# Optimization experiments

Measured on AMD Instinct MI355X. Metric: run time of the kernel, lower is better.

## Reference

```python
import jax, jax.numpy as jnp
import numpy as np

K = 30          # hard-coded in Hypergraph.from_feature_kNN(ft, k=30)
BN_EPS = 1e-5   # BatchNorm1d eval mode, running_mean=0, running_var=1


def setup_inputs() -> dict:
    key = jax.random.key(0)
    ks = jax.random.split(key, 3)
    B, C, H, W = 8, 64, 56, 56
    hid = 32
    return {
        "x": jax.random.normal(ks[0], (B, C, H, W), jnp.float32),
        "w1": jax.random.normal(ks[1], (C, hid), jnp.float32) / np.sqrt(C).astype(np.float32),
        "b1": jnp.zeros((hid,), jnp.float32),
        "g1": jnp.ones((hid,), jnp.float32),
        "be1": jnp.zeros((hid,), jnp.float32),
        "w2": jax.random.normal(ks[2], (hid, C), jnp.float32) / np.sqrt(hid).astype(np.float32),
        "b2": jnp.zeros((C,), jnp.float32),
        "g2": jnp.ones((C,), jnp.float32),
        "be2": jnp.zeros((C,), jnp.float32),
    }


def _knn_idx(ft, k):
    # squared euclidean distances via gram trick; same ordering as torch.cdist
    sq = jnp.sum(ft * ft, axis=1)
    d2 = sq[:, None] + sq[None, :] - 2.0 * (ft @ ft.T)   # [L, L]
    _, idx = jax.lax.top_k(-d2, k)                        # k smallest distances (incl. self)
    return idx                                            # [L, k] -> hyperedge e = kNN of vertex e


def _v2v_mean(X, nbr):
    # hg.v2v(X, aggr="mean"): v2e mean then e2v mean over the kNN incidence structure
    L, k = nbr.shape
    F = X.shape[1]
    Y = jnp.mean(X[nbr], axis=1)                                        # v2e: [L_edges, F]
    seg = nbr.reshape(-1)                                               # vertex nbr[e,j] belongs to edge e
    vals = jnp.broadcast_to(Y[:, None, :], (L, k, F)).reshape(L * k, F)
    s = jax.ops.segment_sum(vals, seg, num_segments=L)                  # e2v sum
    dv = jax.ops.segment_sum(jnp.ones((L * k,), X.dtype), seg, num_segments=L)
    return s / jnp.maximum(dv, 1.0)[:, None]                            # e2v mean


def _bn_eval(x, g, b):
    # BatchNorm1d in eval: running_mean=0, running_var=1
    return x * (g * np.float32(1.0 / np.sqrt(1.0 + BN_EPS))) + b


def reference(x, w1, b1, g1, be1, w2, b2, g2, be2):
    B, C, H, W = x.shape
    L = H * W
    xf = x.reshape(B, L, C)  # faithful raw x.view(B, L, C) (no transpose in source)

    def per_sample(ft):
        nbr = _knn_idx(ft, K)
        # HGNNPConv 1: theta -> bn -> v2v(mean) -> relu (dropout off in eval)
        h = _bn_eval(ft @ w1 + b1, g1, be1)
        h = jax.nn.relu(_v2v_mean(h, nbr))
        # HGNNPConv 2 (is_last): theta -> bn -> v2v(mean), no act/drop
        h = _bn_eval(h @ w2 + b2, g2, be2)
        return _v2v_mean(h, nbr)  # [L, C]

    outs = jax.vmap(per_sample)(xf)      # [B, L, C]
    return outs.reshape(B, -1, H, W)     # faithful raw outs.view(B, -1, H, W)
```

## Files before the change

kernel.cpp:

```cpp
#include <hip/hip_runtime.h>
#include <math.h>


namespace {

constexpr int cB = 8;
constexpr int cL = 3136;
constexpr int cC = 64;
constexpr int cH = 32;
constexpr int cK = 30;
constexpr int NV = cB * cL;
constexpr int QD = 10;
constexpr float BN_SC = 0.99999500003749964f;

typedef __bf16 bf16x4 __attribute__((ext_vector_type(4)));
typedef __bf16 bf16x8 __attribute__((ext_vector_type(8)));
typedef float floatx4 __attribute__((ext_vector_type(4)));

__device__ inline unsigned umin2(unsigned a, unsigned b) { return a < b ? a : b; }
__device__ inline unsigned umax2(unsigned a, unsigned b) { return a > b ? a : b; }
__device__ inline unsigned umin3(unsigned a, unsigned b, unsigned c) {
  return umin2(umin2(a, b), c);
}
__device__ inline float bf16lo(unsigned u) { return __uint_as_float(u << 16); }
__device__ inline float bf16hi(unsigned u) {
  return __uint_as_float(u & 0xFFFF0000u);
}

__device__ inline unsigned bclean64(unsigned v, int ln) {
#pragma unroll
  for (int off = 32; off; off >>= 1) {
    unsigned p = (unsigned)__shfl_xor((int)v, off);
    v = (ln & off) ? umax2(v, p) : umin2(v, p);
  }
  return v;
}

__global__ void k_split(const float* __restrict__ x, ushort* __restrict__ xhi,
                        ushort* __restrict__ xlo, float* __restrict__ sqf,
                        int* __restrict__ cnt, int* __restrict__ cur) {
  int v = blockIdx.x * 256 + threadIdx.x;
  if (v >= NV) return;
  cnt[v] = 0;
  cur[v] = 0;
  const float4* p = reinterpret_cast<const float4*>(x) + (size_t)v * 16;
  double s = 0.0;
#pragma unroll
  for (int c = 0; c < 16; ++c) {
    float4 f = p[c];
    bf16x4 hh, ll;
#pragma unroll
    for (int e = 0; e < 4; ++e) {
      float a = (&f.x)[e];
      __bf16 h = (__bf16)a;
      ll[e] = (__bf16)(a - (float)h);
      hh[e] = h;
      s += (double)a * (double)a;
    }
    *reinterpret_cast<bf16x4*>(&xhi[(size_t)v * 64 + c * 4]) = hh;
    *reinterpret_cast<bf16x4*>(&xlo[(size_t)v * 64 + c * 4]) = ll;
  }
  sqf[v] = (float)(s * 1024.0 + 262144.0);
}

__global__ __launch_bounds__(128, 4) void k_sweep(
    const ushort* __restrict__ xhi, const ushort* __restrict__ xlo,
    const float* __restrict__ sqf, unsigned* __restrict__ candq) {
  const int ib = blockIdx.x, qt = blockIdx.y, b = blockIdx.z;
  const int r0 = ib * 32;
  const int jb0 = qt * 1568;
  const int ntile = 49;
  const size_t bbase = (size_t)b * cL;

  __shared__ ushort aHi[32 * 72], aLo[32 * 72];
  __shared__ ushort bHi[32 * 72], bLo[32 * 72];
  __shared__ float sqJs[32];

  const int t  = threadIdx.x;
  const int ln = t & 63;
  const int w  = t >> 6;
  const int tx = ln & 15;
  const int qd = ln >> 4;

#pragma unroll
  for (int it = 0; it < 2; ++it) {
    int idx = t + 128 * it;
    int r = idx >> 3, blk = idx & 7;
    *reinterpret_cast<uint4*>(&aHi[r * 72 + blk * 8]) =
        *reinterpret_cast<const uint4*>(&xhi[(bbase + r0 + r) * 64 + blk * 8]);
    *reinterpret_cast<uint4*>(&aLo[r * 72 + blk * 8]) =
        *reinterpret_cast<const uint4*>(&xlo[(bbase + r0 + r) * 64 + blk * 8]);
  }
  __syncthreads();

  bf16x8 aH[2], aL[2];
#pragma unroll
  for (int kk = 0; kk < 2; ++kk) {
    aH[kk] = *reinterpret_cast<const bf16x8*>(
        &aHi[(w * 16 + tx) * 72 + kk * 32 + qd * 8]);
    aL[kk] = *reinterpret_cast<const bf16x8*>(
        &aLo[(w * 16 + tx) * 72 + kk * 32 + qd * 8]);
  }

  unsigned q[4][QD];
#pragma unroll
  for (int e = 0; e < 4; ++e)
#pragma unroll
    for (int k = 0; k < QD; ++k) q[e][k] = 0xFFFFFFFFu;

  const int pr  = (t + 0)   >> 3, pblk  = (t + 0)   & 7;
  const int pr1 = (t + 128) >> 3, pblk1 = (t + 128) & 7;
  uint4 pH0, pH1, pL0, pL1;
  float pS = 0.f;
  {
    const int jb = jb0;
    pH0 = *reinterpret_cast<const uint4*>(&xhi[(bbase + jb + pr) * 64 + pblk * 8]);
    pL0 = *reinterpret_cast<const uint4*>(&xlo[(bbase + jb + pr) * 64 + pblk * 8]);
    pH1 = *reinterpret_cast<const uint4*>(&xhi[(bbase + jb + pr1) * 64 + pblk1 * 8]);
    pL1 = *reinterpret_cast<const uint4*>(&xlo[(bbase + jb + pr1) * 64 + pblk1 * 8]);
    if (t < 32) pS = sqf[bbase + jb + t];
  }

  for (int st = 0; st < ntile; ++st) {
    __syncthreads();
    *reinterpret_cast<uint4*>(&bHi[pr * 72 + pblk * 8])   = pH0;
    *reinterpret_cast<uint4*>(&bLo[pr * 72 + pblk * 8])   = pL0;
    *reinterpret_cast<uint4*>(&bHi[pr1 * 72 + pblk1 * 8]) = pH1;
    *reinterpret_cast<uint4*>(&bLo[pr1 * 72 + pblk1 * 8]) = pL1;
    if (t < 32) sqJs[t] = pS;
    __syncthreads();

    if (st + 1 < ntile) {
      const int jb = jb0 + (st + 1) * 32;
      pH0 = *reinterpret_cast<const uint4*>(&xhi[(bbase + jb + pr) * 64 + pblk * 8]);
      pL0 = *reinterpret_cast<const uint4*>(&xlo[(bbase + jb + pr) * 64 + pblk * 8]);
      pH1 = *reinterpret_cast<const uint4*>(&xhi[(bbase + jb + pr1) * 64 + pblk1 * 8]);
      pL1 = *reinterpret_cast<const uint4*>(&xlo[(bbase + jb + pr1) * 64 + pblk1 * 8]);
      if (t < 32) pS = sqf[bbase + jb + t];
    }
    __builtin_amdgcn_sched_barrier(0);

    unsigned pk[2][4];
#pragma unroll
    for (int f = 0; f < 2; ++f) {
      const int bro = (f * 16 + tx) * 72 + qd * 8;
      bf16x8 bh0 = *reinterpret_cast<const bf16x8*>(&bHi[bro]);
      bf16x8 bh1 = *reinterpret_cast<const bf16x8*>(&bHi[bro + 32]);
      bf16x8 bl0 = *reinterpret_cast<const bf16x8*>(&bLo[bro]);
      bf16x8 bl1 = *reinterpret_cast<const bf16x8*>(&bLo[bro + 32]);
      floatx4 acc = {0.f, 0.f, 0.f, 0.f};
      acc = __builtin_amdgcn_mfma_f32_16x16x32_bf16(aH[0], bh0, acc, 0, 0, 0);
      acc = __builtin_amdgcn_mfma_f32_16x16x32_bf16(aH[1], bh1, acc, 0, 0, 0);
      acc = __builtin_amdgcn_mfma_f32_16x16x32_bf16(aH[0], bl0, acc, 0, 0, 0);
      acc = __builtin_amdgcn_mfma_f32_16x16x32_bf16(aH[1], bl1, acc, 0, 0, 0);
      acc = __builtin_amdgcn_mfma_f32_16x16x32_bf16(aL[0], bh0, acc, 0, 0, 0);
      acc = __builtin_amdgcn_mfma_f32_16x16x32_bf16(aL[1], bh1, acc, 0, 0, 0);
      const float sjs = sqJs[f * 16 + tx];
      const unsigned col = (unsigned)(jb0 + st * 32 + f * 16 + tx);
#pragma unroll
      for (int e = 0; e < 4; ++e) {
        float qf = fmaf(acc[e], -2048.f, sjs);
        qf = fminf(fmaxf(qf, 0.f), 1048575.f);
        pk[f][e] = ((unsigned)qf << 12) | col;
      }
    }

#pragma unroll
    for (int e = 0; e < 4; ++e) {
      unsigned a0 = umin2(pk[0][e], pk[1][e]);
      unsigned a1 = umax2(pk[0][e], pk[1][e]);
      if (__any(a0 < q[e][QD - 1])) {
#pragma unroll
        for (int i = QD - 1; i >= 2; --i)
          q[e][i] = umin3(q[e][i], umax2(q[e][i - 1], a0),
                          umax2(q[e][i - 2], a1));
        q[e][1] = umin3(q[e][1], umax2(q[e][0], a0), a1);
        q[e][0] = umin3(q[e][0], a0, a1);
      }
    }
  }

  unsigned* cr[4];
#pragma unroll
  for (int e = 0; e < 4; ++e)
    cr[e] = candq + (bbase + r0 + w * 16 + qd * 4 + e) * 80 + qt * 40;
  for (int it = 0; it < 40; ++it) {
    unsigned h0 = q[0][0], h1 = q[1][0], h2 = q[2][0], h3 = q[3][0];
    unsigned m0 = h0, m1 = h1, m2 = h2, m3 = h3;
#pragma unroll
    for (int off = 1; off < 16; off <<= 1) {
      m0 = umin2(m0, (unsigned)__shfl_xor((int)m0, off));
      m1 = umin2(m1, (unsigned)__shfl_xor((int)m1, off));
      m2 = umin2(m2, (unsigned)__shfl_xor((int)m2, off));
      m3 = umin2(m3, (unsigned)__shfl_xor((int)m3, off));
    }
    if (tx == 0) {
      cr[0][it] = m0;
      cr[1][it] = m1;
      cr[2][it] = m2;
      cr[3][it] = m3;
    }
    if (h0 == m0) {
#pragma unroll
      for (int k = 0; k < QD - 1; ++k) q[0][k] = q[0][k + 1];
      q[0][QD - 1] = 0xFFFFFFFFu;
    }
    if (h1 == m1) {
#pragma unroll
      for (int k = 0; k < QD - 1; ++k) q[1][k] = q[1][k + 1];
      q[1][QD - 1] = 0xFFFFFFFFu;
    }
    if (h2 == m2) {
#pragma unroll
      for (int k = 0; k < QD - 1; ++k) q[2][k] = q[2][k + 1];
      q[2][QD - 1] = 0xFFFFFFFFu;
    }
    if (h3 == m3) {
#pragma unroll
      for (int k = 0; k < QD - 1; ++k) q[3][k] = q[3][k + 1];
      q[3][QD - 1] = 0xFFFFFFFFu;
    }
  }
}

__global__ __launch_bounds__(256) void k_rescore(const float* __restrict__ x,
                                                 const unsigned* __restrict__ candq,
                                                 int* __restrict__ nbr,
                                                 int* __restrict__ cnt) {
  const int w  = threadIdx.x >> 6;
  const int ln = threadIdx.x & 63;
  const size_t row = (size_t)blockIdx.x * 4 + w;
  const size_t bvert = row - (row % cL);

  const unsigned* cq = candq + row * 80;
  unsigned A = (ln < 40) ? cq[ln]      : 0xFFFFFFFFu;
  unsigned B = (ln < 40) ? cq[40 + ln] : 0xFFFFFFFFu;

  unsigned g = umin2(A, (unsigned)__shfl((int)B, 63 - ln));
  g = bclean64(g, ln);

  const unsigned qv = g >> 12;
  const int col = min((int)(g & 0xFFFu), cL - 1);

  unsigned q29 = (unsigned)__shfl((int)qv, 29);
  unsigned q30 = (unsigned)__shfl((int)qv, 30);
  if (q30 > q29 + 6) {
    if (ln < cK) {
      nbr[row * cK + ln] = col;
      atomicAdd(&cnt[bvert + col], 1);
    }
    return;
  }

  float4 xi[16];
  const float4* xi4 = reinterpret_cast<const float4*>(x + row * 64);
#pragma unroll
  for (int c = 0; c < 16; ++c) xi[c] = xi4[c];

  double dv = 1e300;
  if (ln < 40) {
    const float4* xj4 = reinterpret_cast<const float4*>(x + (bvert + col) * 64);
    double ax = 0.0, ay = 0.0, az = 0.0, aw = 0.0;
#pragma unroll
    for (int c = 0; c < 16; ++c) {
      float4 xj = xj4[c];
      double d0 = (double)xi[c].x - (double)xj.x; ax = fma(d0, d0, ax);
      double d1 = (double)xi[c].y - (double)xj.y; ay = fma(d1, d1, ay);
      double d2 = (double)xi[c].z - (double)xj.z; az = fma(d2, d2, az);
      double d3 = (double)xi[c].w - (double)xj.w; aw = fma(d3, d3, aw);
    }
    dv = (ax + ay) + (az + aw);
  }
  int r2 = 0;
  for (int j = 0; j < 40; ++j) {
    double od = __shfl(dv, j);
    r2 += (od < dv || (od == dv && j < ln)) ? 1 : 0;
  }
  if (ln < 40 && r2 < cK) {
    nbr[row * cK + r2] = col;
    atomicAdd(&cnt[bvert + col], 1);
  }
}

__global__ __launch_bounds__(1024) void k_scan(const int* __restrict__ cnt,
                                               int* __restrict__ rp) {
  const int b = blockIdx.x;
  const int* c = cnt + b * cL;
  int* r = rp + b * (cL + 1);
  const int t = threadIdx.x;
  const int ln = t & 63, w = t >> 6;

  int v[4];
  int s = 0;
#pragma unroll
  for (int i = 0; i < 4; ++i) {
    int idx = 4 * t + i;
    v[i] = (idx < cL) ? c[idx] : 0;
    s += v[i];
  }
  int inc = s;
#pragma unroll
  for (int off = 1; off < 64; off <<= 1) {
    int u = __shfl_up(inc, off);
    if (ln >= off) inc += u;
  }
  __shared__ int wsum[16];
  if (ln == 63) wsum[w] = inc;
  __syncthreads();
  int carry = 0;
#pragma unroll
  for (int i = 0; i < 16; ++i) carry += (i < w) ? wsum[i] : 0;

  int excl = carry + inc - s;
#pragma unroll
  for (int i = 0; i < 4; ++i) {
    int idx = 4 * t + i;
    if (idx < cL) r[idx] = excl;
    excl += v[i];
  }
  if (t == 1023) r[cL] = excl;
}

__global__ void k_fill(const int* __restrict__ nbr, const int* __restrict__ rp,
                       int* __restrict__ cur, int* __restrict__ el) {
  int g = blockIdx.x * 256 + threadIdx.x;
  if (g >= NV * cK) return;
  int b = g / (cL * cK);
  int e = (g / cK) % cL;
  int v = nbr[g];
  v = min(max(v, 0), cL - 1);
  int p = rp[b * (cL + 1) + v] + atomicAdd(&cur[b * cL + v], 1);
  p = min(max(p, 0), cL * cK - 1);
  el[(size_t)b * cL * cK + p] = e;
}

__global__ __launch_bounds__(256) void k_theta1(const float* __restrict__ x,
                                                const float* __restrict__ w1,
                                                const float* __restrict__ b1,
                                                const float* __restrict__ g1,
                                                const float* __restrict__ be1,
                                                __bf16* __restrict__ h1) {
  __shared__ float w[cC * cH];
  int t = threadIdx.x;
  for (int n = t; n < cC * cH; n += 256) w[n] = w1[n];
  __syncthreads();
  int g = blockIdx.x * 256 + t;
  int row = g >> 5;
  int f = g & 31;
  const float4* xr = reinterpret_cast<const float4*>(x) + (size_t)row * 16;
  float s = 0.f;
#pragma unroll
  for (int kc = 0; kc < 16; ++kc) {
    float4 xv = xr[kc];
    s += xv.x * w[(4 * kc + 0) * cH + f];
    s += xv.y * w[(4 * kc + 1) * cH + f];
    s += xv.z * w[(4 * kc + 2) * cH + f];
    s += xv.w * w[(4 * kc + 3) * cH + f];
  }
  h1[g] = (__bf16)((s + b1[f]) * (g1[f] * BN_SC) + be1[f]);
}

__global__ __launch_bounds__(256) void k_v2e32(const __bf16* __restrict__ X,
                                               const int* __restrict__ nbr,
                                               __bf16* __restrict__ Y) {
  const int w  = threadIdx.x >> 6;
  const int ln = threadIdx.x & 63;
  const size_t er = (size_t)blockIdx.x * 4 + w;
  const size_t b  = er / cL;
  const unsigned* Xb = reinterpret_cast<const unsigned*>(X + b * cL * cH);
  const int nb_l = nbr[er * cK + (ln < cK ? ln : cK - 1)];
  const int qg = ln >> 4, f2 = ln & 15;
  unsigned u[8];
#pragma unroll
  for (int m = 0; m < 8; ++m) {
    int j = m * 4 + qg;
    int idx = __shfl(nb_l, j < cK ? j : 0);
    u[m] = Xb[(size_t)idx * 16 + f2];
  }
  float s0 = 0.f, s1 = 0.f;
#pragma unroll
  for (int m = 0; m < 8; ++m) {
    bool ok = (m * 4 + qg) < cK;
    s0 += ok ? bf16lo(u[m]) : 0.f;
    s1 += ok ? bf16hi(u[m]) : 0.f;
  }
  s0 += __shfl_xor(s0, 16);
  s1 += __shfl_xor(s1, 16);
  s0 += __shfl_xor(s0, 32);
  s1 += __shfl_xor(s1, 32);
  if (ln < 16) {
    union {
      __bf16 h[2];
      unsigned u;
    } cv;
    cv.h[0] = (__bf16)(s0 * (1.f / 30.f));
    cv.h[1] = (__bf16)(s1 * (1.f / 30.f));
    reinterpret_cast<unsigned*>(Y)[er * 16 + f2] = cv.u;
  }
}

__global__ __launch_bounds__(256) void k_e2v_t2(const __bf16* __restrict__ Y,
                                                const int* __restrict__ rp,
                                                const int* __restrict__ el,
                                                const float* __restrict__ w2,
                                                const float* __restrict__ b2,
                                                const float* __restrict__ g2,
                                                const float* __restrict__ be2,
                                                __bf16* __restrict__ h2) {
  __shared__ float w2s[cH * cC];
  {
    int t = threadIdx.x;
    for (int n = t; n < cH * cC; n += 256) w2s[n] = w2[n];
  }
  const int w  = threadIdx.x >> 6;
  const int ln = threadIdx.x & 63;
  const size_t vr = (size_t)blockIdx.x * 4 + w;
  const size_t b  = vr / cL;
  const int v = (int)(vr % cL);
  const int* rpb = rp + b * (cL + 1);
  const int s0 = rpb[v];
  const int deg = rpb[v + 1] - s0;
  const int* elb = el + b * (size_t)cL * cK + s0;
  const __bf16* Yb = Y + b * cL * cH;
  const int hi = ln >> 5, f = ln & 31;
  float s = 0.f;

  for (int base = 0; base < deg; base += 64) {
    const int take = min(64, deg - base);
    const int eidx = elb[base + (ln < take ? ln : 0)];
    for (int j0 = 0; j0 < take; j0 += 16) {
      float acc = 0.f;
#pragma unroll
      for (int k2 = 0; k2 < 8; ++k2) {
        int j = j0 + 2 * k2 + hi;
        int e0 = __shfl(eidx, j < take ? j : 0);
        float y = (float)Yb[(size_t)e0 * cH + f];
        acc += (j < take) ? y : 0.f;
      }
      s += acc;
    }
  }
  __syncthreads();

  s += __shfl_xor(s, 32);
  float r = fmaxf(s / (float)deg, 0.f);

  float s2 = 0.f;
#pragma unroll 8
  for (int k = 0; k < cH; ++k) {
    float rk = __shfl(r, k);
    s2 = fmaf(rk, w2s[k * cC + ln], s2);
  }
  h2[vr * cC + ln] = (__bf16)((s2 + b2[ln]) * (g2[ln] * BN_SC) + be2[ln]);
}

__global__ __launch_bounds__(256) void k_v2e64(const __bf16* __restrict__ X,
                                               const int* __restrict__ nbr,
                                               __bf16* __restrict__ Y) {
  const int w  = threadIdx.x >> 6;
  const int ln = threadIdx.x & 63;
  const size_t er = (size_t)blockIdx.x * 4 + w;
  const size_t b  = er / cL;
  const unsigned* Xb = reinterpret_cast<const unsigned*>(X + b * cL * cC);
  const int nb_l = nbr[er * cK + (ln < cK ? ln : cK - 1)];
  const int half = ln >> 5, f2 = ln & 31;
  int idx[15];
#pragma unroll
  for (int m = 0; m < 15; ++m) idx[m] = __shfl(nb_l, 2 * m + half);
  unsigned v[15];
#pragma unroll
  for (int m = 0; m < 15; ++m) v[m] = Xb[(size_t)idx[m] * 32 + f2];
  float s0 = 0.f, s1 = 0.f;
#pragma unroll
  for (int m = 0; m < 15; ++m) {
    s0 += bf16lo(v[m]);
    s1 += bf16hi(v[m]);
  }
  s0 += __shfl_xor(s0, 32);
  s1 += __shfl_xor(s1, 32);
  if (half == 0) {
    union {
      __bf16 h[2];
      unsigned u;
    } cv;
    cv.h[0] = (__bf16)(s0 * (1.f / 30.f));
    cv.h[1] = (__bf16)(s1 * (1.f / 30.f));
    reinterpret_cast<unsigned*>(Y)[er * 32 + f2] = cv.u;
  }
}

__global__ __launch_bounds__(256) void k_e2v64(const __bf16* __restrict__ Y,
                                               const int* __restrict__ rp,
                                               const int* __restrict__ el,
                                               float* __restrict__ out) {
  const int w  = threadIdx.x >> 6;
  const int ln = threadIdx.x & 63;
  const size_t vr = (size_t)blockIdx.x * 4 + w;
  const size_t b  = vr / cL;
  const int v = (int)(vr % cL);
  const int* rpb = rp + b * (cL + 1);
  const int s0r = rpb[v];
  const int deg = rpb[v + 1] - s0r;
  const int* elb = el + b * (size_t)cL * cK + s0r;
  const unsigned* Yb = reinterpret_cast<const unsigned*>(Y + b * cL * cC);
  const int half = ln >> 5, f2 = ln & 31;
  float s0 = 0.f, s1 = 0.f;

  for (int base = 0; base < deg; base += 64) {
    const int take = min(64, deg - base);
    const int eidx = elb[base + (ln < take ? ln : 0)];
    for (int j0 = 0; j0 < take; j0 += 16) {
      float a0 = 0.f, a1 = 0.f;
#pragma unroll
      for (int k2 = 0; k2 < 8; ++k2) {
        int j = j0 + 2 * k2 + half;
        int e0 = __shfl(eidx, j < take ? j : 0);
        unsigned u = Yb[(size_t)e0 * 32 + f2];
        bool ok = j < take;
        a0 += ok ? bf16lo(u) : 0.f;
        a1 += ok ? bf16hi(u) : 0.f;
      }
      s0 += a0;
      s1 += a1;
    }
  }
  s0 += __shfl_xor(s0, 32);
  s1 += __shfl_xor(s1, 32);
  float v0 = __shfl(s0, ln >> 1);
  float v1 = __shfl(s1, ln >> 1);
  out[vr * cC + ln] = ((ln & 1) ? v1 : v0) / (float)deg;
}

}

extern "C" void kernel_launch(void* const* d_in, const int* in_sizes, int n_in,
                              void* d_out, int out_size, void* d_ws,
                              size_t ws_size, hipStream_t stream) {
  (void)in_sizes; (void)n_in; (void)out_size; (void)ws_size;
  const float* x   = (const float*)d_in[0];
  const float* w1  = (const float*)d_in[1];
  const float* b1  = (const float*)d_in[2];
  const float* g1  = (const float*)d_in[3];
  const float* be1 = (const float*)d_in[4];
  const float* w2  = (const float*)d_in[5];
  const float* b2  = (const float*)d_in[6];
  const float* g2  = (const float*)d_in[7];
  const float* be2 = (const float*)d_in[8];
  float* out = (float*)d_out;

  char* base = (char*)d_ws;
  size_t off = 0;
  auto carve = [&](size_t bytes) {
    char* p = base + off;
    off += (bytes + 255) & ~(size_t)255;
    return p;
  };
  float* sqf = (float*)carve((size_t)NV * 4);
  int*   nbr = (int*)carve((size_t)NV * cK * 4);
  int*   rp  = (int*)carve((size_t)cB * (cL + 1) * 4);
  int*   cnt = (int*)carve((size_t)NV * 4);
  int*   cur = (int*)carve((size_t)NV * 4);
  char* RA = carve((size_t)NV * 64 * 2 * 2);
  ushort* xhi = (ushort*)RA;
  ushort* xlo = (ushort*)(RA + 3211264);
  int* el = (int*)RA;
  char* RC = carve((size_t)NV * 160 * 4);
  unsigned* candq = (unsigned*)RC;
  __bf16* h1 = (__bf16*)RC;
  __bf16* Y1 = (__bf16*)(RC + 1605632);
  __bf16* h2 = (__bf16*)(RC + 3211264);
  __bf16* Y2 = (__bf16*)(RC + 6422528);

  k_split<<<(NV + 255) / 256, 256, 0, stream>>>(x, xhi, xlo, sqf, cnt, cur);
  k_sweep<<<dim3(98, 2, cB), 128, 0, stream>>>(xhi, xlo, sqf, candq);
  k_rescore<<<NV / 4, 256, 0, stream>>>(x, candq, nbr, cnt);

  k_scan<<<cB, 1024, 0, stream>>>(cnt, rp);
  k_fill<<<(NV * cK) / 256, 256, 0, stream>>>(nbr, rp, cur, el);

  k_theta1<<<NV * cH / 256, 256, 0, stream>>>(x, w1, b1, g1, be1, h1);
  k_v2e32<<<NV / 4, 256, 0, stream>>>(h1, nbr, Y1);
  k_e2v_t2<<<NV / 4, 256, 0, stream>>>(Y1, rp, el, w2, b2, g2, be2, h2);
  k_v2e64<<<NV / 4, 256, 0, stream>>>(h2, nbr, Y2);
  k_e2v64<<<NV / 4, 256, 0, stream>>>(Y2, rp, el, out);
}
```

Before: 389.7 us.

## Fuse split with theta1, fold v2e32 into rescore, drop LDS staging in kNN sweep

```diff
diff --git a/kernel.cpp b/kernel.cpp
--- a/kernel.cpp
+++ b/kernel.cpp
@@ -13,9 +13,13 @@
 constexpr int QD = 10;
 constexpr float BN_SC = 0.99999500003749964f;
 
-typedef __bf16 bf16x4 __attribute__((ext_vector_type(4)));
 typedef __bf16 bf16x8 __attribute__((ext_vector_type(8)));
 typedef float floatx4 __attribute__((ext_vector_type(4)));
+
+union BU {
+  __bf16 b[2];
+  unsigned u;
+};
 
 __device__ inline unsigned umin2(unsigned a, unsigned b) { return a < b ? a : b; }
 __device__ inline unsigned umax2(unsigned a, unsigned b) { return a > b ? a : b; }
@@ -36,71 +40,62 @@
   return v;
 }
 
-__global__ void k_split(const float* __restrict__ x, ushort* __restrict__ xhi,
-                        ushort* __restrict__ xlo, float* __restrict__ sqf,
-                        int* __restrict__ cnt, int* __restrict__ cur) {
-  int v = blockIdx.x * 256 + threadIdx.x;
-  if (v >= NV) return;
-  cnt[v] = 0;
-  cur[v] = 0;
-  const float4* p = reinterpret_cast<const float4*>(x) + (size_t)v * 16;
-  double s = 0.0;
-#pragma unroll
-  for (int c = 0; c < 16; ++c) {
-    float4 f = p[c];
-    bf16x4 hh, ll;
-#pragma unroll
-    for (int e = 0; e < 4; ++e) {
-      float a = (&f.x)[e];
-      __bf16 h = (__bf16)a;
-      ll[e] = (__bf16)(a - (float)h);
-      hh[e] = h;
-      s += (double)a * (double)a;
-    }
-    *reinterpret_cast<bf16x4*>(&xhi[(size_t)v * 64 + c * 4]) = hh;
-    *reinterpret_cast<bf16x4*>(&xlo[(size_t)v * 64 + c * 4]) = ll;
-  }
-  sqf[v] = (float)(s * 1024.0 + 262144.0);
-}
-
-__global__ __launch_bounds__(128, 4) void k_sweep(
+__global__ __launch_bounds__(256) void k_splitth(
+    const float* __restrict__ x, const float* __restrict__ w1,
+    const float* __restrict__ b1, const float* __restrict__ g1,
+    const float* __restrict__ be1, ushort* __restrict__ xhi,
+    ushort* __restrict__ xlo, float* __restrict__ sqf,
+    int* __restrict__ cnt, int* __restrict__ cur, __bf16* __restrict__ h1) {
+  __shared__ float w1s[cC * cH];
+  __shared__ float xs[8 * 64];
+  const int t = threadIdx.x;
+  const int v0 = blockIdx.x * 8;
+  for (int n = t; n < cC * cH; n += 256) w1s[n] = w1[n];
+  {
+    float2 xv = reinterpret_cast<const float2*>(x + (size_t)v0 * 64)[t];
+    xs[2 * t] = xv.x;
+    xs[2 * t + 1] = xv.y;
+    BU hh, ll;
+    hh.b[0] = (__bf16)xv.x;
+    hh.b[1] = (__bf16)xv.y;
+    ll.b[0] = (__bf16)(xv.x - (float)hh.b[0]);
+    ll.b[1] = (__bf16)(xv.y - (float)hh.b[1]);
+    reinterpret_cast<unsigned*>(xhi)[(size_t)v0 * 32 + t] = hh.u;
+    reinterpret_cast<unsigned*>(xlo)[(size_t)v0 * 32 + t] = ll.u;
+    float ss = xv.x * xv.x + xv.y * xv.y;
+#pragma unroll
+    for (int off = 1; off < 32; off <<= 1) ss += __shfl_xor(ss, off);
+    if ((t & 31) == 0) sqf[v0 + (t >> 5)] = ss * 1024.f + 262144.f;
+  }
+  if (t < 8) {
+    cnt[v0 + t] = 0;
+    cur[v0 + t] = 0;
+  }
+  __syncthreads();
+  const int r = t >> 5, f = t & 31;
+  float s = 0.f;
+#pragma unroll
+  for (int k = 0; k < cC; ++k) s = fmaf(xs[r * 64 + k], w1s[k * cH + f], s);
+  h1[(size_t)(v0 + r) * cH + f] =
+      (__bf16)((s + b1[f]) * (g1[f] * BN_SC) + be1[f]);
+}
+
+__global__ __launch_bounds__(64, 4) void k_sweep(
     const ushort* __restrict__ xhi, const ushort* __restrict__ xlo,
     const float* __restrict__ sqf, unsigned* __restrict__ candq) {
   const int ib = blockIdx.x, qt = blockIdx.y, b = blockIdx.z;
-  const int r0 = ib * 32;
+  const int r0 = ib * 16;
   const int jb0 = qt * 1568;
-  const int ntile = 49;
   const size_t bbase = (size_t)b * cL;
-
-  __shared__ ushort aHi[32 * 72], aLo[32 * 72];
-  __shared__ ushort bHi[32 * 72], bLo[32 * 72];
-  __shared__ float sqJs[32];
-
-  const int t  = threadIdx.x;
-  const int ln = t & 63;
-  const int w  = t >> 6;
+  const int ln = threadIdx.x;
   const int tx = ln & 15;
   const int qd = ln >> 4;
 
-#pragma unroll
-  for (int it = 0; it < 2; ++it) {
-    int idx = t + 128 * it;
-    int r = idx >> 3, blk = idx & 7;
-    *reinterpret_cast<uint4*>(&aHi[r * 72 + blk * 8]) =
-        *reinterpret_cast<const uint4*>(&xhi[(bbase + r0 + r) * 64 + blk * 8]);
-    *reinterpret_cast<uint4*>(&aLo[r * 72 + blk * 8]) =
-        *reinterpret_cast<const uint4*>(&xlo[(bbase + r0 + r) * 64 + blk * 8]);
-  }
-  __syncthreads();
-
-  bf16x8 aH[2], aL[2];
-#pragma unroll
-  for (int kk = 0; kk < 2; ++kk) {
-    aH[kk] = *reinterpret_cast<const bf16x8*>(
-        &aHi[(w * 16 + tx) * 72 + kk * 32 + qd * 8]);
-    aL[kk] = *reinterpret_cast<const bf16x8*>(
-        &aLo[(w * 16 + tx) * 72 + kk * 32 + qd * 8]);
-  }
+  const size_t aoff = (bbase + r0 + tx) * 64 + qd * 8;
+  const bf16x8 aH0 = *reinterpret_cast<const bf16x8*>(&xhi[aoff]);
+  const bf16x8 aH1 = *reinterpret_cast<const bf16x8*>(&xhi[aoff + 32]);
+  const bf16x8 aL0 = *reinterpret_cast<const bf16x8*>(&xlo[aoff]);
+  const bf16x8 aL1 = *reinterpret_cast<const bf16x8*>(&xlo[aoff + 32]);
 
   unsigned q[4][QD];
 #pragma unroll
@@ -108,82 +103,70 @@
 #pragma unroll
     for (int k = 0; k < QD; ++k) q[e][k] = 0xFFFFFFFFu;
 
-  const int pr  = (t + 0)   >> 3, pblk  = (t + 0)   & 7;
-  const int pr1 = (t + 128) >> 3, pblk1 = (t + 128) & 7;
-  uint4 pH0, pH1, pL0, pL1;
-  float pS = 0.f;
-  {
-    const int jb = jb0;
-    pH0 = *reinterpret_cast<const uint4*>(&xhi[(bbase + jb + pr) * 64 + pblk * 8]);
-    pL0 = *reinterpret_cast<const uint4*>(&xlo[(bbase + jb + pr) * 64 + pblk * 8]);
-    pH1 = *reinterpret_cast<const uint4*>(&xhi[(bbase + jb + pr1) * 64 + pblk1 * 8]);
-    pL1 = *reinterpret_cast<const uint4*>(&xlo[(bbase + jb + pr1) * 64 + pblk1 * 8]);
-    if (t < 32) pS = sqf[bbase + jb + t];
-  }
-
-  for (int st = 0; st < ntile; ++st) {
-    __syncthreads();
-    *reinterpret_cast<uint4*>(&bHi[pr * 72 + pblk * 8])   = pH0;
-    *reinterpret_cast<uint4*>(&bLo[pr * 72 + pblk * 8])   = pL0;
-    *reinterpret_cast<uint4*>(&bHi[pr1 * 72 + pblk1 * 8]) = pH1;
-    *reinterpret_cast<uint4*>(&bLo[pr1 * 72 + pblk1 * 8]) = pL1;
-    if (t < 32) sqJs[t] = pS;
-    __syncthreads();
-
-    if (st + 1 < ntile) {
-      const int jb = jb0 + (st + 1) * 32;
-      pH0 = *reinterpret_cast<const uint4*>(&xhi[(bbase + jb + pr) * 64 + pblk * 8]);
-      pL0 = *reinterpret_cast<const uint4*>(&xlo[(bbase + jb + pr) * 64 + pblk * 8]);
-      pH1 = *reinterpret_cast<const uint4*>(&xhi[(bbase + jb + pr1) * 64 + pblk1 * 8]);
-      pL1 = *reinterpret_cast<const uint4*>(&xlo[(bbase + jb + pr1) * 64 + pblk1 * 8]);
-      if (t < 32) pS = sqf[bbase + jb + t];
-    }
-    __builtin_amdgcn_sched_barrier(0);
-
-    unsigned pk[2][4];
-#pragma unroll
-    for (int f = 0; f < 2; ++f) {
-      const int bro = (f * 16 + tx) * 72 + qd * 8;
-      bf16x8 bh0 = *reinterpret_cast<const bf16x8*>(&bHi[bro]);
-      bf16x8 bh1 = *reinterpret_cast<const bf16x8*>(&bHi[bro + 32]);
-      bf16x8 bl0 = *reinterpret_cast<const bf16x8*>(&bLo[bro]);
-      bf16x8 bl1 = *reinterpret_cast<const bf16x8*>(&bLo[bro + 32]);
-      floatx4 acc = {0.f, 0.f, 0.f, 0.f};
-      acc = __builtin_amdgcn_mfma_f32_16x16x32_bf16(aH[0], bh0, acc, 0, 0, 0);
-      acc = __builtin_amdgcn_mfma_f32_16x16x32_bf16(aH[1], bh1, acc, 0, 0, 0);
-      acc = __builtin_amdgcn_mfma_f32_16x16x32_bf16(aH[0], bl0, acc, 0, 0, 0);
-      acc = __builtin_amdgcn_mfma_f32_16x16x32_bf16(aH[1], bl1, acc, 0, 0, 0);
-      acc = __builtin_amdgcn_mfma_f32_16x16x32_bf16(aL[0], bh0, acc, 0, 0, 0);
-      acc = __builtin_amdgcn_mfma_f32_16x16x32_bf16(aL[1], bh1, acc, 0, 0, 0);
-      const float sjs = sqJs[f * 16 + tx];
-      const unsigned col = (unsigned)(jb0 + st * 32 + f * 16 + tx);
-#pragma unroll
-      for (int e = 0; e < 4; ++e) {
-        float qf = fmaf(acc[e], -2048.f, sjs);
-        qf = fminf(fmaxf(qf, 0.f), 1048575.f);
-        pk[f][e] = ((unsigned)qf << 12) | col;
-      }
-    }
-
+  const ushort* ph0 = xhi + (bbase + jb0 + tx) * 64 + qd * 8;
+  const ushort* ph1 = ph0 + 16 * 64;
+  const ushort* pl0 = xlo + (bbase + jb0 + tx) * 64 + qd * 8;
+  const ushort* pl1 = pl0 + 16 * 64;
+  const float* ps = sqf + bbase + jb0 + tx;
+
+  for (int st = 0; st < 49; ++st) {
+    bf16x8 b0h0 = *reinterpret_cast<const bf16x8*>(ph0);
+    bf16x8 b0h1 = *reinterpret_cast<const bf16x8*>(ph0 + 32);
+    bf16x8 b0l0 = *reinterpret_cast<const bf16x8*>(pl0);
+    bf16x8 b0l1 = *reinterpret_cast<const bf16x8*>(pl0 + 32);
+    bf16x8 b1h0 = *reinterpret_cast<const bf16x8*>(ph1);
+    bf16x8 b1h1 = *reinterpret_cast<const bf16x8*>(ph1 + 32);
+    bf16x8 b1l0 = *reinterpret_cast<const bf16x8*>(pl1);
+    bf16x8 b1l1 = *reinterpret_cast<const bf16x8*>(pl1 + 32);
+    const float sj0 = ps[0];
+    const float sj1 = ps[16];
+
+    floatx4 acc0 = {0.f, 0.f, 0.f, 0.f};
+    acc0 = __builtin_amdgcn_mfma_f32_16x16x32_bf16(aH0, b0h0, acc0, 0, 0, 0);
+    acc0 = __builtin_amdgcn_mfma_f32_16x16x32_bf16(aH1, b0h1, acc0, 0, 0, 0);
+    acc0 = __builtin_amdgcn_mfma_f32_16x16x32_bf16(aH0, b0l0, acc0, 0, 0, 0);
+    acc0 = __builtin_amdgcn_mfma_f32_16x16x32_bf16(aH1, b0l1, acc0, 0, 0, 0);
+    acc0 = __builtin_amdgcn_mfma_f32_16x16x32_bf16(aL0, b0h0, acc0, 0, 0, 0);
+    acc0 = __builtin_amdgcn_mfma_f32_16x16x32_bf16(aL1, b0h1, acc0, 0, 0, 0);
+    floatx4 acc1 = {0.f, 0.f, 0.f, 0.f};
+    acc1 = __builtin_amdgcn_mfma_f32_16x16x32_bf16(aH0, b1h0, acc1, 0, 0, 0);
+    acc1 = __builtin_amdgcn_mfma_f32_16x16x32_bf16(aH1, b1h1, acc1, 0, 0, 0);
+    acc1 = __builtin_amdgcn_mfma_f32_16x16x32_bf16(aH0, b1l0, acc1, 0, 0, 0);
+    acc1 = __builtin_amdgcn_mfma_f32_16x16x32_bf16(aH1, b1l1, acc1, 0, 0, 0);
+    acc1 = __builtin_amdgcn_mfma_f32_16x16x32_bf16(aL0, b1h0, acc1, 0, 0, 0);
+    acc1 = __builtin_amdgcn_mfma_f32_16x16x32_bf16(aL1, b1h1, acc1, 0, 0, 0);
+
+    const unsigned col0 = (unsigned)(jb0 + st * 32 + tx);
+    unsigned pk0[4], pk1[4];
 #pragma unroll
     for (int e = 0; e < 4; ++e) {
-      unsigned a0 = umin2(pk[0][e], pk[1][e]);
-      unsigned a1 = umax2(pk[0][e], pk[1][e]);
-      if (__any(a0 < q[e][QD - 1])) {
-#pragma unroll
-        for (int i = QD - 1; i >= 2; --i)
-          q[e][i] = umin3(q[e][i], umax2(q[e][i - 1], a0),
-                          umax2(q[e][i - 2], a1));
-        q[e][1] = umin3(q[e][1], umax2(q[e][0], a0), a1);
-        q[e][0] = umin3(q[e][0], a0, a1);
-      }
-    }
+      float q0 = fmaf(acc0[e], -2048.f, sj0);
+      q0 = fminf(fmaxf(q0, 0.f), 1048575.f);
+      pk0[e] = ((unsigned)q0 << 12) | col0;
+      float q1 = fmaf(acc1[e], -2048.f, sj1);
+      q1 = fminf(fmaxf(q1, 0.f), 1048575.f);
+      pk1[e] = ((unsigned)q1 << 12) | (col0 + 16);
+    }
+
+#pragma unroll
+    for (int e = 0; e < 4; ++e) {
+      unsigned a0 = umin2(pk0[e], pk1[e]);
+      unsigned a1 = umax2(pk0[e], pk1[e]);
+#pragma unroll
+      for (int i = QD - 1; i >= 2; --i)
+        q[e][i] = umin3(q[e][i], umax2(q[e][i - 1], a0),
+                        umax2(q[e][i - 2], a1));
+      q[e][1] = umin3(q[e][1], umax2(q[e][0], a0), a1);
+      q[e][0] = umin3(q[e][0], a0, a1);
+    }
+
+    ph0 += 2048; ph1 += 2048; pl0 += 2048; pl1 += 2048; ps += 32;
   }
 
   unsigned* cr[4];
 #pragma unroll
   for (int e = 0; e < 4; ++e)
-    cr[e] = candq + (bbase + r0 + w * 16 + qd * 4 + e) * 80 + qt * 40;
+    cr[e] = candq + (bbase + r0 + qd * 4 + e) * 80 + qt * 40;
   for (int it = 0; it < 40; ++it) {
     unsigned h0 = q[0][0], h1 = q[1][0], h2 = q[2][0], h3 = q[3][0];
     unsigned m0 = h0, m1 = h1, m2 = h2, m3 = h3;
@@ -223,10 +206,10 @@
   }
 }
 
-__global__ __launch_bounds__(256) void k_rescore(const float* __restrict__ x,
-                                                 const unsigned* __restrict__ candq,
-                                                 int* __restrict__ nbr,
-                                                 int* __restrict__ cnt) {
+__global__ __launch_bounds__(256) void k_rescore(
+    const float* __restrict__ x, const unsigned* __restrict__ candq,
+    const __bf16* __restrict__ h1, int* __restrict__ nbr,
+    int* __restrict__ cnt, __bf16* __restrict__ Y1) {
   const int w  = threadIdx.x >> 6;
   const int ln = threadIdx.x & 63;
   const size_t row = (size_t)blockIdx.x * 4 + w;
@@ -244,41 +227,60 @@
 
   unsigned q29 = (unsigned)__shfl((int)qv, 29);
   unsigned q30 = (unsigned)__shfl((int)qv, 30);
-  if (q30 > q29 + 6) {
-    if (ln < cK) {
-      nbr[row * cK + ln] = col;
-      atomicAdd(&cnt[bvert + col], 1);
-    }
-    return;
-  }
-
-  float4 xi[16];
-  const float4* xi4 = reinterpret_cast<const float4*>(x + row * 64);
-#pragma unroll
-  for (int c = 0; c < 16; ++c) xi[c] = xi4[c];
-
-  double dv = 1e300;
-  if (ln < 40) {
-    const float4* xj4 = reinterpret_cast<const float4*>(x + (bvert + col) * 64);
-    double ax = 0.0, ay = 0.0, az = 0.0, aw = 0.0;
-#pragma unroll
-    for (int c = 0; c < 16; ++c) {
-      float4 xj = xj4[c];
-      double d0 = (double)xi[c].x - (double)xj.x; ax = fma(d0, d0, ax);
-      double d1 = (double)xi[c].y - (double)xj.y; ay = fma(d1, d1, ay);
-      double d2 = (double)xi[c].z - (double)xj.z; az = fma(d2, d2, az);
-      double d3 = (double)xi[c].w - (double)xj.w; aw = fma(d3, d3, aw);
-    }
-    dv = (ax + ay) + (az + aw);
-  }
-  int r2 = 0;
-  for (int j = 0; j < 40; ++j) {
-    double od = __shfl(dv, j);
-    r2 += (od < dv || (od == dv && j < ln)) ? 1 : 0;
-  }
-  if (ln < 40 && r2 < cK) {
-    nbr[row * cK + r2] = col;
-    atomicAdd(&cnt[bvert + col], 1);
+  int myc = col;
+  if (!(q30 > q29 + 6)) {
+    float4 xi[16];
+    const float4* xi4 = reinterpret_cast<const float4*>(x + row * 64);
+#pragma unroll
+    for (int c = 0; c < 16; ++c) xi[c] = xi4[c];
+    double dv = 1e300;
+    if (ln < 40) {
+      const float4* xj4 =
+          reinterpret_cast<const float4*>(x + (bvert + col) * 64);
+      double ax = 0.0, ay = 0.0, az = 0.0, aw = 0.0;
+#pragma unroll
+      for (int c = 0; c < 16; ++c) {
+        float4 xj = xj4[c];
+        double d0 = (double)xi[c].x - (double)xj.x; ax = fma(d0, d0, ax);
+        double d1 = (double)xi[c].y - (double)xj.y; ay = fma(d1, d1, ay);
+        double d2 = (double)xi[c].z - (double)xj.z; az = fma(d2, d2, az);
+        double d3 = (double)xi[c].w - (double)xj.w; aw = fma(d3, d3, aw);
+      }
+      dv = (ax + ay) + (az + aw);
+    }
+    int r2 = 0;
+    for (int j = 0; j < 40; ++j) {
+      double od = __shfl(dv, j);
+      r2 += (od < dv || (od == dv && j < ln)) ? 1 : 0;
+    }
+    myc = __builtin_amdgcn_ds_permute(r2 << 2, col);
+  }
+  if (ln < cK) {
+    nbr[row * cK + ln] = myc;
+    atomicAdd(&cnt[bvert + myc], 1);
+  }
+
+  const unsigned* Xb = reinterpret_cast<const unsigned*>(h1 + bvert * cH);
+  const int qg = ln >> 4, f2 = ln & 15;
+  float s0 = 0.f, s1 = 0.f;
+#pragma unroll
+  for (int m = 0; m < 8; ++m) {
+    int j = m * 4 + qg;
+    int idx = __shfl(myc, j < cK ? j : 0);
+    unsigned u = Xb[(size_t)idx * 16 + f2];
+    bool ok = j < cK;
+    s0 += ok ? bf16lo(u) : 0.f;
+    s1 += ok ? bf16hi(u) : 0.f;
+  }
+  s0 += __shfl_xor(s0, 16);
+  s1 += __shfl_xor(s1, 16);
+  s0 += __shfl_xor(s0, 32);
+  s1 += __shfl_xor(s1, 32);
+  if (ln < 16) {
+    BU cv;
+    cv.b[0] = (__bf16)(s0 * (1.f / 30.f));
+    cv.b[1] = (__bf16)(s1 * (1.f / 30.f));
+    reinterpret_cast<unsigned*>(Y1)[row * 16 + f2] = cv.u;
   }
 }
 
@@ -332,71 +334,6 @@
   int p = rp[b * (cL + 1) + v] + atomicAdd(&cur[b * cL + v], 1);
   p = min(max(p, 0), cL * cK - 1);
   el[(size_t)b * cL * cK + p] = e;
-}
-
-__global__ __launch_bounds__(256) void k_theta1(const float* __restrict__ x,
-                                                const float* __restrict__ w1,
-                                                const float* __restrict__ b1,
-                                                const float* __restrict__ g1,
-                                                const float* __restrict__ be1,
-                                                __bf16* __restrict__ h1) {
-  __shared__ float w[cC * cH];
-  int t = threadIdx.x;
-  for (int n = t; n < cC * cH; n += 256) w[n] = w1[n];
-  __syncthreads();
-  int g = blockIdx.x * 256 + t;
-  int row = g >> 5;
-  int f = g & 31;
-  const float4* xr = reinterpret_cast<const float4*>(x) + (size_t)row * 16;
-  float s = 0.f;
-#pragma unroll
-  for (int kc = 0; kc < 16; ++kc) {
-    float4 xv = xr[kc];
-    s += xv.x * w[(4 * kc + 0) * cH + f];
-    s += xv.y * w[(4 * kc + 1) * cH + f];
-    s += xv.z * w[(4 * kc + 2) * cH + f];
-    s += xv.w * w[(4 * kc + 3) * cH + f];
-  }
-  h1[g] = (__bf16)((s + b1[f]) * (g1[f] * BN_SC) + be1[f]);
-}
-
-__global__ __launch_bounds__(256) void k_v2e32(const __bf16* __restrict__ X,
-                                               const int* __restrict__ nbr,
-                                               __bf16* __restrict__ Y) {
-  const int w  = threadIdx.x >> 6;
-  const int ln = threadIdx.x & 63;
-  const size_t er = (size_t)blockIdx.x * 4 + w;
-  const size_t b  = er / cL;
-  const unsigned* Xb = reinterpret_cast<const unsigned*>(X + b * cL * cH);
-  const int nb_l = nbr[er * cK + (ln < cK ? ln : cK - 1)];
-  const int qg = ln >> 4, f2 = ln & 15;
-  unsigned u[8];
-#pragma unroll
-  for (int m = 0; m < 8; ++m) {
-    int j = m * 4 + qg;
-    int idx = __shfl(nb_l, j < cK ? j : 0);
-    u[m] = Xb[(size_t)idx * 16 + f2];
-  }
-  float s0 = 0.f, s1 = 0.f;
-#pragma unroll
-  for (int m = 0; m < 8; ++m) {
-    bool ok = (m * 4 + qg) < cK;
-    s0 += ok ? bf16lo(u[m]) : 0.f;
-    s1 += ok ? bf16hi(u[m]) : 0.f;
-  }
-  s0 += __shfl_xor(s0, 16);
-  s1 += __shfl_xor(s1, 16);
-  s0 += __shfl_xor(s0, 32);
-  s1 += __shfl_xor(s1, 32);
-  if (ln < 16) {
-    union {
-      __bf16 h[2];
-      unsigned u;
-    } cv;
-    cv.h[0] = (__bf16)(s0 * (1.f / 30.f));
-    cv.h[1] = (__bf16)(s1 * (1.f / 30.f));
-    reinterpret_cast<unsigned*>(Y)[er * 16 + f2] = cv.u;
-  }
 }
 
 __global__ __launch_bounds__(256) void k_e2v_t2(const __bf16* __restrict__ Y,
@@ -479,12 +416,9 @@
   s0 += __shfl_xor(s0, 32);
   s1 += __shfl_xor(s1, 32);
   if (half == 0) {
-    union {
-      __bf16 h[2];
-      unsigned u;
-    } cv;
-    cv.h[0] = (__bf16)(s0 * (1.f / 30.f));
-    cv.h[1] = (__bf16)(s1 * (1.f / 30.f));
+    BU cv;
+    cv.b[0] = (__bf16)(s0 * (1.f / 30.f));
+    cv.b[1] = (__bf16)(s1 * (1.f / 30.f));
     reinterpret_cast<unsigned*>(Y)[er * 32 + f2] = cv.u;
   }
 }
@@ -564,22 +498,21 @@
   ushort* xhi = (ushort*)RA;
   ushort* xlo = (ushort*)(RA + 3211264);
   int* el = (int*)RA;
-  char* RC = carve((size_t)NV * 160 * 4);
+  char* RC = carve(17661952);
   unsigned* candq = (unsigned*)RC;
-  __bf16* h1 = (__bf16*)RC;
-  __bf16* Y1 = (__bf16*)(RC + 1605632);
-  __bf16* h2 = (__bf16*)(RC + 3211264);
-  __bf16* Y2 = (__bf16*)(RC + 6422528);
-
-  k_split<<<(NV + 255) / 256, 256, 0, stream>>>(x, xhi, xlo, sqf, cnt, cur);
-  k_sweep<<<dim3(98, 2, cB), 128, 0, stream>>>(xhi, xlo, sqf, candq);
-  k_rescore<<<NV / 4, 256, 0, stream>>>(x, candq, nbr, cnt);
+  __bf16* h1 = (__bf16*)(RC + 8028160);
+  __bf16* Y1 = (__bf16*)(RC + 9633792);
+  __bf16* h2 = (__bf16*)(RC + 11239424);
+  __bf16* Y2 = (__bf16*)(RC + 14450688);
+
+  k_splitth<<<NV / 8, 256, 0, stream>>>(x, w1, b1, g1, be1, xhi, xlo, sqf,
+                                        cnt, cur, h1);
+  k_sweep<<<dim3(196, 2, cB), 64, 0, stream>>>(xhi, xlo, sqf, candq);
+  k_rescore<<<NV / 4, 256, 0, stream>>>(x, candq, h1, nbr, cnt, Y1);
 
   k_scan<<<cB, 1024, 0, stream>>>(cnt, rp);
   k_fill<<<(NV * cK) / 256, 256, 0, stream>>>(nbr, rp, cur, el);
 
-  k_theta1<<<NV * cH / 256, 256, 0, stream>>>(x, w1, b1, g1, be1, h1);
-  k_v2e32<<<NV / 4, 256, 0, stream>>>(h1, nbr, Y1);
   k_e2v_t2<<<NV / 4, 256, 0, stream>>>(Y1, rp, el, w2, b2, g2, be2, h2);
   k_v2e64<<<NV / 4, 256, 0, stream>>>(h2, nbr, Y2);
   k_e2v64<<<NV / 4, 256, 0, stream>>>(Y2, rp, el, out);
```

After: 437.1 us. 12.1% more time.
